# Kernel tuning notes

Hardware: AMD Instinct MI355X
Metric: run time of the kernel (lower is better)

Reference implementation:

```python
import jax, jax.numpy as jnp
import numpy as np
from jax.scipy.special import logsumexp

K = 15          # top-k
N = 4096        # n candidates
BS = 128        # batch size
EPS = 0.1       # entropic regularizer epsilon
MAX_ITER = 200  # Sinkhorn iterations
RANK = 5        # rank of pseudoinverse init
SMALL = 1e-20


def _build_weights():
    """Rank-5 pseudoinverse of Sinkhorn constraint matrix A (as in __init__).
    A maps (f in R^n, g in R^k) -> (f_i + g_c) over rows r = i*(k+1)+c (g_k := 0).
    A^T A = [[(k+1) I_n, J_{n x k}], [J_{k x n}, n I_k]] in closed form."""
    k1 = K + 1
    p = N + K
    G = np.zeros((p, p), dtype=np.float64)
    G[:N, :N] = (k1) * np.eye(N)
    G[:N, N:] = 1.0
    G[N:, :N] = 1.0
    G[N:, N:] = N * np.eye(K)
    w, V = np.linalg.eigh(G)
    idx = np.argsort(w)[-RANK:]
    s = np.sqrt(w[idx])
    V = V[:, idx]                                  # (p, RANK)
    # U = A @ V / s without materializing A (1GB dense):
    vf = V[:N]                                     # (N, RANK)
    vg = np.concatenate([V[N:], np.zeros((1, RANK))], axis=0)  # (k1, RANK)
    U = (vf[:, None, :] + vg[None, :, :]).reshape(N * k1, RANK) / s
    weight1 = (V / s).astype(np.float32)           # (N+K, RANK) = V diag(1/s)
    weight2 = U.T.astype(np.float32)               # (RANK, N*(K+1)) = U^T
    return jnp.asarray(weight1), jnp.asarray(weight2)


def setup_inputs() -> dict:
    key = jax.random.key(0)
    scores = jax.random.normal(key, (BS, N), dtype=jnp.float32)
    tau = jnp.ones((1,), jnp.float32) * 0.1
    weight1, weight2 = _build_weights()
    return {"scores": scores, "tau": tau, "weight1": weight1, "weight2": weight2}


def _sinkhorn(C, mu, nu, Gamma0, weight1, weight2):
    bs, n, k1 = C.shape
    # least-squares warm start for potentials f, g
    b = (C + EPS * jnp.log(Gamma0)).reshape(bs, -1)          # (bs, n*k1)
    x = jnp.einsum('bm,rm->br', b, weight2)                  # (bs, RANK)
    x = jnp.einsum('br,pr->bp', x, weight1)                  # (bs, n+k)
    f = x[:, :n, None]                                       # (bs, n, 1)
    g = jnp.concatenate([x[:, n:], jnp.zeros((bs, 1), C.dtype)], axis=-1)[:, None, :]  # (bs,1,k1)
    elog_mu = EPS * jnp.log(mu)                              # (1, n, 1)
    elog_nu = EPS * jnp.log(nu)                              # (1, 1, k1)

    def step(carry, _):
        f, g = carry
        f = -EPS * logsumexp(-(C - g) / EPS, axis=-1, keepdims=True) + elog_mu
        g = -EPS * logsumexp(-(C - f) / EPS, axis=-2, keepdims=True) + elog_nu
        return (f, g), None

    (f, g), _ = jax.lax.scan(step, (f, g), None, length=MAX_ITER)
    return jnp.exp((-C + f + g) / EPS)


def reference(scores, tau, weight1, weight2):
    bs, n = scores.shape
    k = K
    s = scores[:, :, None]                                   # (bs, n, 1)
    sd = jax.lax.stop_gradient(s)
    max_s = jnp.max(sd)
    min_s = jnp.min(jnp.where(jnp.isneginf(sd), jnp.inf, sd))
    filled = min_s - (max_s - min_s)
    s = jnp.where(jnp.isneginf(s), filled, s)
    anchors = jnp.arange(k, -1, -1, dtype=s.dtype).reshape(1, 1, k + 1)
    C = (s - anchors) ** 2
    C = C / jax.lax.stop_gradient(C.max())
    mu = jnp.full((1, n, 1), 1.0 / n, dtype=s.dtype)
    nu = jnp.concatenate([jnp.full((k,), 1.0 / n), jnp.array([(n - k) / n])]).astype(s.dtype).reshape(1, 1, k + 1)
    # warm-start transport plan Gamma0 from (detached) hard top-k
    topk_val = jax.lax.top_k(jax.lax.stop_gradient(s[..., 0]), k)[0]      # (bs, k)
    Gamma0 = jax.nn.sigmoid(-jnp.abs(topk_val[:, None, :] - s) / tau)     # (bs, n, k)
    Gamma0 = Gamma0 + SMALL
    Gamma0 = Gamma0 / Gamma0.sum(-2, keepdims=True) / n
    Gamma0_last = jnp.clip(1.0 / n - Gamma0.sum(-1, keepdims=True), SMALL, 1.0 - SMALL)
    Gamma0 = jnp.concatenate([Gamma0, Gamma0_last], axis=-1)              # (bs, n, k+1)
    Gamma = _sinkhorn(C, mu, nu, Gamma0, weight1, weight2)
    A = Gamma[:, :, :k] * n
    return A, jnp.linalg.norm(Gamma - Gamma0)
```

## Files before the change

kernel.cpp:

```cpp
#include <hip/hip_runtime.h>
#include <math.h>

#define KK 15
#define K1 16
#define NN 4096
#define BSZ 128
#define NT 512
#define RPT 8
#define NPAIR 4
#define NW 8
#define EPSI 0.1f
#define SMALLC 1e-20f
#define NITER 100
#define W2STRIDE 65536
#define OUT_A_ELEMS (BSZ * NN * KK)
#define TS 20
#define CONV_REL 2e-6f

typedef __attribute__((ext_vector_type(2))) float f2;
typedef __attribute__((ext_vector_type(2))) unsigned u2v;
__device__ __forceinline__ f2 pk_fma(f2 a, f2 b, f2 c){
  return __builtin_elementwise_fma(a, b, c);
}

__device__ __forceinline__ unsigned enc_f32(float f){
  unsigned u = __float_as_uint(f);
  return (u & 0x80000000u) ? ~u : (u | 0x80000000u);
}
__device__ __forceinline__ float dec_f32(unsigned e){
  unsigned u = (e & 0x80000000u) ? (e ^ 0x80000000u) : ~e;
  return __uint_as_float(u);
}


template<int CTRL>
__device__ __forceinline__ float dpp_movf(float x){
  return __uint_as_float((unsigned)__builtin_amdgcn_update_dpp(
      (int)0, (int)__float_as_uint(x), CTRL, 0xF, 0xF, true));
}

__device__ __forceinline__ float bcast_lane0(float x){
  return __uint_as_float((unsigned)__builtin_amdgcn_readlane(
      (int)__float_as_uint(x), 0));
}

__device__ __forceinline__ float xsum16(float r){
#if __has_builtin(__builtin_amdgcn_permlane16_swap)
  u2v s = __builtin_amdgcn_permlane16_swap(__float_as_uint(r), __float_as_uint(r), false, false);
  return __uint_as_float(s.x) + __uint_as_float(s.y);
#else
  return r + __shfl_xor(r, 16);
#endif
}
__device__ __forceinline__ float xsum32(float r){
#if __has_builtin(__builtin_amdgcn_permlane32_swap)
  u2v s = __builtin_amdgcn_permlane32_swap(__float_as_uint(r), __float_as_uint(r), false, false);
  return __uint_as_float(s.x) + __uint_as_float(s.y);
#else
  return r + __shfl_xor(r, 32);
#endif
}

__device__ __forceinline__ float sum16_all(float v){
  v += dpp_movf<0x128>(v);
  v += dpp_movf<0x124>(v);
  v += dpp_movf<0x4E>(v);
  v += dpp_movf<0xB1>(v);
  return v;
}

__device__ __forceinline__ float full64_sum(float v){
  return xsum32(xsum16(sum16_all(v)));
}

__device__ __forceinline__ int fold_col(int lane){
  int l = lane & 15;
  return ((l & 1) << 3) | ((l & 2) << 1) | ((l & 8) >> 2) | ((l & 4) >> 2);
}

__device__ __forceinline__ float wave_fold16(const float p[K1], int lane){
  float a[8];
  {
    const bool hi = (lane & 1) != 0;
    #pragma unroll
    for (int j = 0; j < 8; ++j){
      float send = hi ? p[j] : p[j + 8];
      float keep = hi ? p[j + 8] : p[j];
      a[j] = keep + dpp_movf<0xB1>(send);
    }
  }
  float bq[4];
  {
    const bool hi = (lane & 2) != 0;
    #pragma unroll
    for (int j = 0; j < 4; ++j){
      float send = hi ? a[j] : a[j + 4];
      float keep = hi ? a[j + 4] : a[j];
      bq[j] = keep + dpp_movf<0x4E>(send);
    }
  }
  float cq[2];
  {
    const bool hi = (lane & 8) != 0;
    float s0 = hi ? bq[0] : bq[2];
    float s1 = hi ? bq[1] : bq[3];
    float k0 = hi ? bq[2] : bq[0];
    float k1 = hi ? bq[3] : bq[1];
    cq[0] = k0 + dpp_movf<0x128>(s0);
    cq[1] = k1 + dpp_movf<0x128>(s1);
  }
  float r;
  {
    const bool hi = (lane & 4) != 0;
    float send = hi ? cq[0] : cq[1];
    float keep = hi ? cq[1] : cq[0];
    r = keep + __shfl_xor(send, 4);
  }
  r = xsum16(r);
  r = xsum32(r);
  return r;
}

__device__ __forceinline__ void block_fold16(const float p[K1], float* wb, float* tb,
                                             int lane, int wv, int tid){
  float r = wave_fold16(p, lane);
  if (lane < 16) wb[wv * K1 + fold_col(lane)] = r;
  __syncthreads();
  if (tid < 16){
    float t = 0.0f;
    #pragma unroll
    for (int q = 0; q < NW; ++q) t += wb[q * K1 + tid];
    tb[tid] = t;
  }
  __syncthreads();
}

__global__ __launch_bounds__(NT, 2) void k_main(
    const float* __restrict__ scores, const float* __restrict__ taup,
    const float* __restrict__ w1, const float* __restrict__ w2,
    float* __restrict__ out, unsigned* __restrict__ ws){
  const int b = blockIdx.x;
  const int tid = threadIdx.x;
  const int lane = tid & 63;
  const int wv = tid >> 6;

  __shared__ float tk[KK];
  __shared__ float cands[NW * KK];
  __shared__ __align__(16) float cbuf[K1];
  __shared__ float wbuf[NW * K1];
  __shared__ float wrow[NW * 5];
  __shared__ __align__(16) float xbuf[K1];
  __shared__ __align__(16) float bbcol[K1];
  __shared__ float xv5[8];
  __shared__ __align__(16) float wbufT[2][K1 * TS];
  __shared__ float rv[NW];
  __shared__ float rmn[NW];
  __shared__ unsigned sng[NW];
  __shared__ float statb[4];

  float raw[RPT];
  #pragma unroll
  for (int j = 0; j < RPT; ++j) raw[j] = scores[(size_t)b * NN + tid + NT * j];

  {
    float mx = -INFINITY, mn = INFINITY; unsigned neg = 0u;
    #pragma unroll
    for (int j = 0; j < RPT; ++j){
      float v = raw[j];
      mx = fmaxf(mx, v);
      if (v == -INFINITY) neg = 1u; else mn = fminf(mn, v);
    }
    #pragma unroll
    for (int off = 32; off; off >>= 1){
      mx = fmaxf(mx, __shfl_xor(mx, off));
      mn = fminf(mn, __shfl_xor(mn, off));
      neg |= (unsigned)__shfl_xor((int)neg, off);
    }
    if (lane == 0){ rv[wv] = mx; rmn[wv] = mn; sng[wv] = neg; }
    __syncthreads();
    if (tid == 0){
      for (int q = 1; q < NW; ++q){
        mx = fmaxf(mx, rv[q]); mn = fminf(mn, rmn[q]); neg |= sng[q];
      }
      atomicMax(&ws[0], enc_f32(mx));
      atomicMax(&ws[5], ~enc_f32(mn));
      if (neg) atomicOr(&ws[1], 1u);
      __threadfence();
      atomicAdd(&ws[3], 1u);
      while (__hip_atomic_load(&ws[3], __ATOMIC_ACQUIRE, __HIP_MEMORY_SCOPE_AGENT) < (unsigned)BSZ)
        __builtin_amdgcn_s_sleep(2);
      statb[0] = dec_f32(__hip_atomic_load(&ws[0], __ATOMIC_RELAXED, __HIP_MEMORY_SCOPE_AGENT));
      statb[1] = dec_f32(~__hip_atomic_load(&ws[5], __ATOMIC_RELAXED, __HIP_MEMORY_SCOPE_AGENT));
      statb[2] = __hip_atomic_load(&ws[1], __ATOMIC_RELAXED, __HIP_MEMORY_SCOPE_AGENT) ? 1.0f : 0.0f;
    }
    __syncthreads();
  }

  const float smax = statb[0];
  const float smin_raw = statb[1];
  const bool has_neg = statb[2] != 0.0f;
  const float filled = smin_raw - (smax - smin_raw);
  const float smin_eff = has_neg ? filled : smin_raw;
  const float cmax = fmaxf(fmaxf(smin_eff * smin_eff, smax * smax),
                           fmaxf((smin_eff - 15.0f) * (smin_eff - 15.0f),
                                 (smax - 15.0f) * (smax - 15.0f)));
  const float cinv = 1.0f / cmax;
  const float tauv = taup[0];
  const float invtau = 1.0f / tauv;
  const float inv_n = 1.0f / (float)NN;

  float sv[RPT];
  #pragma unroll
  for (int j = 0; j < RPT; ++j){
    float v = raw[j]; if (v == -INFINITY) v = filled;
    sv[j] = v;
  }

  {
    float lv[RPT];
    #pragma unroll
    for (int j = 0; j < RPT; ++j) lv[j] = sv[j];
    #pragma unroll
    for (int t = 0; t < KK; ++t){
      float bv = lv[0]; int bs = 0;
      #pragma unroll
      for (int j = 1; j < RPT; ++j){ if (lv[j] > bv){ bv = lv[j]; bs = j; } }
      int bidx = (lane << 3) | bs;
      #pragma unroll
      for (int off = 32; off; off >>= 1){
        float ov = __shfl_xor(bv, off);
        int oi = __shfl_xor(bidx, off);
        if (ov > bv || (ov == bv && oi < bidx)){ bv = ov; bidx = oi; }
      }
      if ((bidx >> 3) == lane){
        int s = bidx & 7;
        #pragma unroll
        for (int j = 0; j < RPT; ++j) if (j == s) lv[j] = -INFINITY;
      }
      if (lane == 0) cands[wv * KK + t] = bv;
    }
  }
  __syncthreads();
  if (wv == 0){
    float c0 = (lane < NW * KK) ? cands[lane] : -INFINITY;
    float c1 = (lane + 64 < NW * KK) ? cands[lane + 64] : -INFINITY;
    #pragma unroll
    for (int t = 0; t < KK; ++t){
      int sel = (c0 >= c1) ? 0 : 1;
      float bv = sel ? c1 : c0;
      int bidx = (lane << 1) | sel;
      #pragma unroll
      for (int off = 32; off; off >>= 1){
        float ov = __shfl_xor(bv, off);
        int oi = __shfl_xor(bidx, off);
        if (ov > bv || (ov == bv && oi < bidx)){ bv = ov; bidx = oi; }
      }
      if ((bidx >> 1) == lane){
        if ((bidx & 1) == 0) c0 = -INFINITY; else c1 = -INFINITY;
      }
      if (lane == 0) tk[t] = bv;
    }
  }
  __syncthreads();

  {
    float p[K1];
    float tkr[KK];
    #pragma unroll
    for (int c = 0; c < KK; ++c) tkr[c] = tk[c];
    #pragma unroll
    for (int c = 0; c < K1; ++c) p[c] = 0.0f;
    #pragma unroll
    for (int j = 0; j < RPT; ++j){
      float si = sv[j];
      #pragma unroll
      for (int c = 0; c < KK; ++c){
        float z = fabsf(tkr[c] - si) * invtau;
        float raw1 = __builtin_amdgcn_rcpf(1.0f + __expf(z)) + SMALLC;
        p[c] += raw1;
      }
    }
    block_fold16(p, wbuf, cbuf, lane, wv, tid);
  }

  float colinv_n[KK];
  {
    float pcol[K1];
    float pr0 = 0.0f, pr1 = 0.0f, pr2 = 0.0f, pr3 = 0.0f, pr4 = 0.0f;
    float tkr[KK];
    #pragma unroll
    for (int c = 0; c < KK; ++c){
      tkr[c] = tk[c];
      colinv_n[c] = (1.0f / cbuf[c]) * inv_n;
    }
    #pragma unroll
    for (int c = 0; c < K1; ++c) pcol[c] = 0.0f;
    #pragma unroll
    for (int j = 0; j < RPT; ++j){
      int i = tid + NT * j;
      float si = sv[j];
      float bb[K1];
      float rowpart = 0.0f;
      #pragma unroll
      for (int c = 0; c < KK; ++c){
        float d = si - (float)(KK - c);
        float Cc = d * d * cinv;
        float z = fabsf(tkr[c] - si) * invtau;
        float raw1 = __builtin_amdgcn_rcpf(1.0f + __expf(z)) + SMALLC;
        float g0 = raw1 * colinv_n[c];
        rowpart += g0;
        bb[c] = Cc + EPSI * __logf(g0);
      }
      {
        float Cc = si * si * cinv;
        float g0l = fminf(fmaxf(inv_n - rowpart, SMALLC), 1.0f - SMALLC);
        bb[KK] = Cc + EPSI * __logf(g0l);
      }
      float rs = 0.0f;
      #pragma unroll
      for (int c = 0; c < K1; ++c){ pcol[c] += bb[c]; rs += bb[c]; }
      const float* w1r = w1 + (size_t)i * 5;
      pr0 = fmaf(w1r[0], rs, pr0);
      pr1 = fmaf(w1r[1], rs, pr1);
      pr2 = fmaf(w1r[2], rs, pr2);
      pr3 = fmaf(w1r[3], rs, pr3);
      pr4 = fmaf(w1r[4], rs, pr4);
    }
    float rcol = wave_fold16(pcol, lane);
    float r0 = full64_sum(pr0);
    float r1 = full64_sum(pr1);
    float r2 = full64_sum(pr2);
    float r3 = full64_sum(pr3);
    float r4 = full64_sum(pr4);
    if (lane < 16) wbuf[wv * K1 + fold_col(lane)] = rcol;
    if (lane == 16) wrow[wv * 5 + 0] = r0;
    if (lane == 17) wrow[wv * 5 + 1] = r1;
    if (lane == 18) wrow[wv * 5 + 2] = r2;
    if (lane == 19) wrow[wv * 5 + 3] = r3;
    if (lane == 20) wrow[wv * 5 + 4] = r4;
    __syncthreads();
    if (tid < 16){
      float t = 0.0f;
      #pragma unroll
      for (int q = 0; q < NW; ++q) t += wbuf[q * K1 + tid];
      bbcol[tid] = t;
    } else if (tid < 21){
      int r = tid - 16;
      float t = 0.0f;
      #pragma unroll
      for (int q = 0; q < NW; ++q) t += wrow[q * 5 + r];
      xbuf[r] = t;
    }
    __syncthreads();
    if (tid < 5){
      float xr = xbuf[tid];
      #pragma unroll
      for (int c = 0; c < KK; ++c)
        xr = fmaf(w1[(size_t)(NN + c) * 5 + tid], bbcol[c], xr);
      xv5[tid] = xr;
    }
    __syncthreads();
  }

  float vt[K1];
  {
    float xv[5];
    #pragma unroll
    for (int r = 0; r < 5; ++r) xv[r] = xv5[r];
    #pragma unroll
    for (int c = 0; c < KK; ++c){
      float g = 0.0f;
      #pragma unroll
      for (int r = 0; r < 5; ++r) g += xv[r] * w1[(size_t)(NN + c) * 5 + r];
      float Bc = expf(-10.0f * cinv * (float)((KK - c) * (KK - c)));
      vt[c] = Bc * expf(g * 10.0f);
    }
    vt[KK] = 1.0f;
  }

  f2 x2[NPAIR];
  #pragma unroll
  for (int q = 0; q < NPAIR; ++q){
    x2[q].x = expf(sv[2 * q] * (-20.0f * cinv));
    x2[q].y = expf(sv[2 * q + 1] * (-20.0f * cinv));
  }
  f2 xp[NPAIR][K1];
  #pragma unroll
  for (int q = 0; q < NPAIR; ++q){
    xp[q][0].x = 1.0f; xp[q][0].y = 1.0f;
    xp[q][1] = x2[q];
    #pragma unroll
    for (int c = 2; c < K1; ++c) xp[q][c] = xp[q][c - 1] * x2[q];
  }

  f2 t2[NPAIR];
  const float nmul = ((lane & 15) < KK) ? 1.0f : 4081.0f;
  float pv2 = 0.0f, pv1 = 0.0f;
  int pcnt = -1;
  #pragma unroll 1
  for (int it = 0; it < NITER; ++it){
    const int ph = it & 1;
    #pragma unroll
    for (int q = 0; q < NPAIR; ++q){
      f2 h; h.x = vt[KK]; h.y = vt[KK];
      #pragma unroll
      for (int c = KK - 1; c >= 0; --c){
        f2 vc; vc.x = vt[c]; vc.y = vt[c];
        h = pk_fma(h, x2[q], vc);
      }
      t2[q].x = __builtin_amdgcn_rcpf(h.x);
      t2[q].y = __builtin_amdgcn_rcpf(h.y);
    }
    float p[K1];
    #pragma unroll
    for (int c = 0; c < K1; ++c){
      f2 s = t2[0] * xp[0][c];
      #pragma unroll
      for (int q = 1; q < NPAIR; ++q) s = pk_fma(t2[q], xp[q][c], s);
      p[c] = s.x + s.y;
    }
    float r = wave_fold16(p, lane);
    if (lane < 16) wbufT[ph][fold_col(lane) * TS + wv] = r;
    __syncthreads();
    float md = -1.0f;
    float wout = 0.0f;
    if (lane < 16){
      const float* wp = &wbufT[ph][lane * TS];
      float4 a4 = *(const float4*)wp;
      float4 b4 = *(const float4*)(wp + 4);
      float t = ((a4.x + a4.y) + (a4.z + a4.w)) + ((b4.x + b4.y) + (b4.z + b4.w));
      float wnew = nmul * __builtin_amdgcn_rcpf(t);
      md = fabsf(wnew - pv1) - CONV_REL * pv1;
      wout = wnew;
    }
    if (pcnt >= 1){
      float r1 = 0.0f, r2 = 0.0f;
      if (lane < 16){
        float winv = __builtin_amdgcn_rcpf(wout);
        r1 = (pv1 - pv2) * winv;
        r2 = (wout - pv1) * winv;
      }
      float s12 = full64_sum(r1 * r2);
      float s11 = full64_sum(r1 * r1);
      float s12b = bcast_lane0(s12);
      float s11b = bcast_lane0(s11);
      int anymove = __any((lane < 16) && (fabsf(r2) > 4.0f * CONV_REL));
      float fac = s12b * __builtin_amdgcn_rcpf(s11b - s12b);
      float acc = wout * (1.0f + r2 * fac);
      int okbr = (lane < 16) ? (acc > 0.1f * wout && acc < 10.0f * wout) : 1;
      int allbr = __all(okbr);
      if ((s12b > 0.0f) && (s12b < 0.97f * s11b) && anymove && allbr){
        if (lane < 16) wout = acc;
        pcnt = -1;
      }
    }
    pcnt++;
    pv2 = pv1; pv1 = wout;
    int conv = __all(md <= 0.0f);
    #pragma unroll
    for (int c = 0; c < K1; ++c)
      vt[c] = __uint_as_float((unsigned)__builtin_amdgcn_readlane(
                  (int)__float_as_uint(wout), c));
    if (conv) break;
  }

  float nrm = 0.0f;
  {
    float tkr[KK];
    #pragma unroll
    for (int c = 0; c < KK; ++c) tkr[c] = tk[c];
    #pragma unroll
    for (int q = 0; q < NPAIR; ++q){
      #pragma unroll
      for (int half = 0; half < 2; ++half){
        int i = tid + NT * (2 * q + half);
        float si = sv[2 * q + half];
        float tin = (half ? t2[q].y : t2[q].x) * inv_n;
        float rowpart = 0.0f;
        float gamv[KK];
        float gaml;
        #pragma unroll
        for (int c = 0; c < KK; ++c){
          float xc = half ? xp[q][c].y : xp[q][c].x;
          float gam = (tin * xc) * vt[c];
          float z = fabsf(tkr[c] - si) * invtau;
          float raw1 = __builtin_amdgcn_rcpf(1.0f + __expf(z)) + SMALLC;
          float g0 = raw1 * colinv_n[c];
          rowpart += g0;
          float d = gam - g0;
          nrm += d * d;
          gamv[c] = gam * (float)NN;
        }
        {
          float xc = half ? xp[q][KK].y : xp[q][KK].x;
          gaml = (tin * xc) * vt[KK];
          float g0l = fminf(fmaxf(inv_n - rowpart, SMALLC), 1.0f - SMALLC);
          float d = gaml - g0l;
          nrm += d * d;
        }
        float* op = out + (size_t)(b * NN + i) * KK;
        #pragma unroll
        for (int c = 0; c < KK; ++c) op[c] = gamv[c];
      }
    }
  }
  #pragma unroll
  for (int off = 32; off; off >>= 1) nrm += __shfl_xor(nrm, off);
  if (lane == 0) rv[wv] = nrm;
  __syncthreads();
  if (tid == 0){
    float t = 0.0f;
    for (int q = 0; q < NW; ++q) t += rv[q];
    atomicAdd(reinterpret_cast<float*>(ws) + 2, t);
    __threadfence();
    unsigned prev = atomicAdd(&ws[4], 1u);
    if (prev == (unsigned)(BSZ - 1)){
      float n2 = __hip_atomic_load(reinterpret_cast<float*>(ws) + 2,
                                   __ATOMIC_RELAXED, __HIP_MEMORY_SCOPE_AGENT);
      out[OUT_A_ELEMS] = sqrtf(n2);
    }
  }
}

extern "C" void kernel_launch(void* const* d_in, const int* in_sizes, int n_in,
                              void* d_out, int out_size, void* d_ws, size_t ws_size,
                              hipStream_t stream){
  const float* scores = (const float*)d_in[0];
  const float* tau    = (const float*)d_in[1];
  const float* w1     = (const float*)d_in[2];
  const float* w2     = (const float*)d_in[3];
  float* out = (float*)d_out;
  unsigned* ws = (unsigned*)d_ws;

  hipMemsetAsync(ws, 0x00, 24, stream);

  k_main<<<BSZ, NT, 0, stream>>>(scores, tau, w1, w2, out, ws);
}
```

Before: 142.4 us.

## Split each batch row across two cooperating blocks with pairwise global syncs

Launches two blocks per batch row instead of one. Each block handles half the candidate rows in the top-k, warm-start column sums and output-writing phases. Partial top-k lists, column sums and least-squares reductions are merged through per-row workspace slots using a global-memory pair barrier. The Sinkhorn iteration itself still appears to run redundantly in both blocks. The change adds cross-block spin waits and relies on all 256 blocks being co-resident for the global statistics barrier.

```diff
diff --git a/kernel.cpp b/kernel.cpp
--- a/kernel.cpp
+++ b/kernel.cpp
@@ -5,17 +5,28 @@
 #define K1 16
 #define NN 4096
 #define BSZ 128
+#define NBLK 256
 #define NT 512
 #define RPT 8
+#define RPTD 4
 #define NPAIR 4
 #define NW 8
 #define EPSI 0.1f
 #define SMALLC 1e-20f
 #define NITER 100
-#define W2STRIDE 65536
 #define OUT_A_ELEMS (BSZ * NN * KK)
 #define TS 20
 #define CONV_REL 2e-6f
+
+#define SLOTW 128
+#define WS_WORDS (16 + BSZ * SLOTW)
+#define SO_CTOP 0
+#define SO_CCOL 1
+#define SO_CWARM 2
+#define SO_TOPK 8
+#define SO_COL  40
+#define SO_WCOL 72
+#define SO_RD   104
 
 typedef __attribute__((ext_vector_type(2))) float f2;
 typedef __attribute__((ext_vector_type(2))) unsigned u2v;
@@ -31,7 +42,6 @@
   unsigned u = (e & 0x80000000u) ? (e ^ 0x80000000u) : ~e;
   return __uint_as_float(u);
 }
-
 
 template<int CTRL>
 __device__ __forceinline__ float dpp_movf(float x){
@@ -68,7 +78,6 @@
   v += dpp_movf<0xB1>(v);
   return v;
 }
-
 __device__ __forceinline__ float full64_sum(float v){
   return xsum32(xsum16(sum16_all(v)));
 }
@@ -135,14 +144,30 @@
   __syncthreads();
 }
 
+__device__ __forceinline__ void pair_sync(unsigned* ctr, int tid){
+  __threadfence();
+  __syncthreads();
+  if (tid == 0){
+    __hip_atomic_fetch_add(ctr, 1u, __ATOMIC_RELEASE, __HIP_MEMORY_SCOPE_AGENT);
+    while (__hip_atomic_load(ctr, __ATOMIC_ACQUIRE, __HIP_MEMORY_SCOPE_AGENT) < 2u)
+      __builtin_amdgcn_s_sleep(1);
+  }
+  __syncthreads();
+}
+
 __global__ __launch_bounds__(NT, 2) void k_main(
     const float* __restrict__ scores, const float* __restrict__ taup,
     const float* __restrict__ w1, const float* __restrict__ w2,
     float* __restrict__ out, unsigned* __restrict__ ws){
-  const int b = blockIdx.x;
+  const int bid = blockIdx.x;
+  const int b   = bid & (BSZ - 1);
+  const int half= bid >> 7;
+  const int JB  = 4 * half;
   const int tid = threadIdx.x;
   const int lane = tid & 63;
   const int wv = tid >> 6;
+  unsigned* slot = ws + 16 + b * SLOTW;
+  float* slotf = (float*)slot;
 
   __shared__ float tk[KK];
   __shared__ float cands[NW * KK];
@@ -187,7 +212,7 @@
       if (neg) atomicOr(&ws[1], 1u);
       __threadfence();
       atomicAdd(&ws[3], 1u);
-      while (__hip_atomic_load(&ws[3], __ATOMIC_ACQUIRE, __HIP_MEMORY_SCOPE_AGENT) < (unsigned)BSZ)
+      while (__hip_atomic_load(&ws[3], __ATOMIC_ACQUIRE, __HIP_MEMORY_SCOPE_AGENT) < (unsigned)NBLK)
         __builtin_amdgcn_s_sleep(2);
       statb[0] = dec_f32(__hip_atomic_load(&ws[0], __ATOMIC_RELAXED, __HIP_MEMORY_SCOPE_AGENT));
       statb[1] = dec_f32(~__hip_atomic_load(&ws[5], __ATOMIC_RELAXED, __HIP_MEMORY_SCOPE_AGENT));
@@ -217,25 +242,25 @@
   }
 
   {
-    float lv[RPT];
-    #pragma unroll
-    for (int j = 0; j < RPT; ++j) lv[j] = sv[j];
+    float lv[RPTD];
+    #pragma unroll
+    for (int j = 0; j < RPTD; ++j) lv[j] = sv[JB + j];
     #pragma unroll
     for (int t = 0; t < KK; ++t){
       float bv = lv[0]; int bs = 0;
       #pragma unroll
-      for (int j = 1; j < RPT; ++j){ if (lv[j] > bv){ bv = lv[j]; bs = j; } }
-      int bidx = (lane << 3) | bs;
+      for (int j = 1; j < RPTD; ++j){ if (lv[j] > bv){ bv = lv[j]; bs = j; } }
+      int bidx = (lane << 2) | bs;
       #pragma unroll
       for (int off = 32; off; off >>= 1){
         float ov = __shfl_xor(bv, off);
         int oi = __shfl_xor(bidx, off);
         if (ov > bv || (ov == bv && oi < bidx)){ bv = ov; bidx = oi; }
       }
-      if ((bidx >> 3) == lane){
-        int s = bidx & 7;
+      if ((bidx >> 2) == lane){
+        int s = bidx & 3;
         #pragma unroll
-        for (int j = 0; j < RPT; ++j) if (j == s) lv[j] = -INFINITY;
+        for (int j = 0; j < RPTD; ++j) if (j == s) lv[j] = -INFINITY;
       }
       if (lane == 0) cands[wv * KK + t] = bv;
     }
@@ -262,6 +287,19 @@
     }
   }
   __syncthreads();
+  if (tid < K1) slotf[SO_TOPK + half * K1 + tid] = (tid < KK) ? tk[tid] : -INFINITY;
+  pair_sync(&slot[SO_CTOP], tid);
+  if (tid == 0){
+    const float* ga = slotf + SO_TOPK;
+    const float* gb = slotf + SO_TOPK + K1;
+    int ia = 0, ib = 0;
+    #pragma unroll
+    for (int t = 0; t < KK; ++t){
+      float va = ga[ia], vb = gb[ib];
+      if (va >= vb){ tk[t] = va; ++ia; } else { tk[t] = vb; ++ib; }
+    }
+  }
+  __syncthreads();
 
   {
     float p[K1];
@@ -271,8 +309,8 @@
     #pragma unroll
     for (int c = 0; c < K1; ++c) p[c] = 0.0f;
     #pragma unroll
-    for (int j = 0; j < RPT; ++j){
-      float si = sv[j];
+    for (int j = 0; j < RPTD; ++j){
+      float si = sv[JB + j];
       #pragma unroll
       for (int c = 0; c < KK; ++c){
         float z = fabsf(tkr[c] - si) * invtau;
@@ -282,6 +320,10 @@
     }
     block_fold16(p, wbuf, cbuf, lane, wv, tid);
   }
+  if (tid < K1) slotf[SO_COL + half * K1 + tid] = cbuf[tid];
+  pair_sync(&slot[SO_CCOL], tid);
+  if (tid < K1) cbuf[tid] = slotf[SO_COL + tid] + slotf[SO_COL + K1 + tid];
+  __syncthreads();
 
   float colinv_n[KK];
   {
@@ -296,9 +338,9 @@
     #pragma unroll
     for (int c = 0; c < K1; ++c) pcol[c] = 0.0f;
     #pragma unroll
-    for (int j = 0; j < RPT; ++j){
-      int i = tid + NT * j;
-      float si = sv[j];
+    for (int j = 0; j < RPTD; ++j){
+      int i = tid + NT * (JB + j);
+      float si = sv[JB + j];
       float bb[K1];
       float rowpart = 0.0f;
       #pragma unroll
@@ -352,6 +394,15 @@
       xbuf[r] = t;
     }
     __syncthreads();
+    if (tid < K1) slotf[SO_WCOL + half * K1 + tid] = bbcol[tid];
+    else if (tid < K1 + 5) slotf[SO_RD + half * 8 + (tid - K1)] = xbuf[tid - K1];
+    pair_sync(&slot[SO_CWARM], tid);
+    if (tid < K1) bbcol[tid] = slotf[SO_WCOL + tid] + slotf[SO_WCOL + K1 + tid];
+    else if (tid < K1 + 5){
+      int r = tid - K1;
+      xbuf[r] = slotf[SO_RD + r] + slotf[SO_RD + 8 + r];
+    }
+    __syncthreads();
     if (tid < 5){
       float xr = xbuf[tid];
       #pragma unroll
@@ -470,18 +521,19 @@
     #pragma unroll
     for (int c = 0; c < KK; ++c) tkr[c] = tk[c];
     #pragma unroll
-    for (int q = 0; q < NPAIR; ++q){
-      #pragma unroll
-      for (int half = 0; half < 2; ++half){
-        int i = tid + NT * (2 * q + half);
-        float si = sv[2 * q + half];
-        float tin = (half ? t2[q].y : t2[q].x) * inv_n;
+    for (int qq = 0; qq < 2; ++qq){
+      const int q = 2 * half + qq;
+      #pragma unroll
+      for (int e = 0; e < 2; ++e){
+        int i = tid + NT * (2 * q + e);
+        float si = sv[2 * q + e];
+        float tin = (e ? t2[q].y : t2[q].x) * inv_n;
         float rowpart = 0.0f;
         float gamv[KK];
         float gaml;
         #pragma unroll
         for (int c = 0; c < KK; ++c){
-          float xc = half ? xp[q][c].y : xp[q][c].x;
+          float xc = e ? xp[q][c].y : xp[q][c].x;
           float gam = (tin * xc) * vt[c];
           float z = fabsf(tkr[c] - si) * invtau;
           float raw1 = __builtin_amdgcn_rcpf(1.0f + __expf(z)) + SMALLC;
@@ -492,7 +544,7 @@
           gamv[c] = gam * (float)NN;
         }
         {
-          float xc = half ? xp[q][KK].y : xp[q][KK].x;
+          float xc = e ? xp[q][KK].y : xp[q][KK].x;
           gaml = (tin * xc) * vt[KK];
           float g0l = fminf(fmaxf(inv_n - rowpart, SMALLC), 1.0f - SMALLC);
           float d = gaml - g0l;
@@ -514,7 +566,7 @@
     atomicAdd(reinterpret_cast<float*>(ws) + 2, t);
     __threadfence();
     unsigned prev = atomicAdd(&ws[4], 1u);
-    if (prev == (unsigned)(BSZ - 1)){
+    if (prev == (unsigned)(NBLK - 1)){
       float n2 = __hip_atomic_load(reinterpret_cast<float*>(ws) + 2,
                                    __ATOMIC_RELAXED, __HIP_MEMORY_SCOPE_AGENT);
       out[OUT_A_ELEMS] = sqrtf(n2);
@@ -532,7 +584,7 @@
   float* out = (float*)d_out;
   unsigned* ws = (unsigned*)d_ws;
 
-  hipMemsetAsync(ws, 0x00, 24, stream);
-
-  k_main<<<BSZ, NT, 0, stream>>>(scores, tau, w1, w2, out, ws);
-}
+  hipMemsetAsync(ws, 0x00, WS_WORDS * 4, stream);
+
+  k_main<<<NBLK, NT, 0, stream>>>(scores, tau, w1, w2, out, ws);
+}
```

Measured after the change: 269.0 us. 1.89x slower.

## Duplicate each batch row across two blocks and overlap top-k with grid barrier

Applied to the files above, without the earlier changes.

Launches two blocks per batch row. Both blocks redundantly run the full Sinkhorn iteration, and each writes half of the output rows and half of the norm contribution. The per-row top-k selection now runs before the global min/max spin-wait, so it overlaps the grid-wide barrier, and -inf top-k values are replaced by the fill value afterwards. This doubles the Sinkhorn compute and relies on all 256 blocks being co-resident for the spin barrier, in exchange for splitting the heavy output-write epilogue and filling more CUs.

```diff
diff --git a/kernel.cpp b/kernel.cpp
--- a/kernel.cpp
+++ b/kernel.cpp
@@ -5,6 +5,7 @@
 #define K1 16
 #define NN 4096
 #define BSZ 128
+#define NBLK 256
 #define NT 512
 #define RPT 8
 #define NPAIR 4
@@ -12,7 +13,6 @@
 #define EPSI 0.1f
 #define SMALLC 1e-20f
 #define NITER 100
-#define W2STRIDE 65536
 #define OUT_A_ELEMS (BSZ * NN * KK)
 #define TS 20
 #define CONV_REL 2e-6f
@@ -68,7 +68,6 @@
   v += dpp_movf<0xB1>(v);
   return v;
 }
-
 __device__ __forceinline__ float full64_sum(float v){
   return xsum32(xsum16(sum16_all(v)));
 }
@@ -139,7 +138,9 @@
     const float* __restrict__ scores, const float* __restrict__ taup,
     const float* __restrict__ w1, const float* __restrict__ w2,
     float* __restrict__ out, unsigned* __restrict__ ws){
-  const int b = blockIdx.x;
+  const int bid = blockIdx.x;
+  const int b   = bid & (BSZ - 1);
+  const int half= bid >> 7;
   const int tid = threadIdx.x;
   const int lane = tid & 63;
   const int wv = tid >> 6;
@@ -187,14 +188,62 @@
       if (neg) atomicOr(&ws[1], 1u);
       __threadfence();
       atomicAdd(&ws[3], 1u);
-      while (__hip_atomic_load(&ws[3], __ATOMIC_ACQUIRE, __HIP_MEMORY_SCOPE_AGENT) < (unsigned)BSZ)
-        __builtin_amdgcn_s_sleep(2);
-      statb[0] = dec_f32(__hip_atomic_load(&ws[0], __ATOMIC_RELAXED, __HIP_MEMORY_SCOPE_AGENT));
-      statb[1] = dec_f32(~__hip_atomic_load(&ws[5], __ATOMIC_RELAXED, __HIP_MEMORY_SCOPE_AGENT));
-      statb[2] = __hip_atomic_load(&ws[1], __ATOMIC_RELAXED, __HIP_MEMORY_SCOPE_AGENT) ? 1.0f : 0.0f;
-    }
-    __syncthreads();
-  }
+    }
+  }
+
+  {
+    float lv[RPT];
+    #pragma unroll
+    for (int j = 0; j < RPT; ++j) lv[j] = raw[j];
+    #pragma unroll
+    for (int t = 0; t < KK; ++t){
+      float bv = lv[0]; int bs = 0;
+      #pragma unroll
+      for (int j = 1; j < RPT; ++j){ if (lv[j] > bv){ bv = lv[j]; bs = j; } }
+      int bidx = (lane << 3) | bs;
+      #pragma unroll
+      for (int off = 32; off; off >>= 1){
+        float ov = __shfl_xor(bv, off);
+        int oi = __shfl_xor(bidx, off);
+        if (ov > bv || (ov == bv && oi < bidx)){ bv = ov; bidx = oi; }
+      }
+      if ((bidx >> 3) == lane){
+        int s = bidx & 7;
+        #pragma unroll
+        for (int j = 0; j < RPT; ++j) if (j == s) lv[j] = -INFINITY;
+      }
+      if (lane == 0) cands[wv * KK + t] = bv;
+    }
+  }
+  __syncthreads();
+  if (wv == 0){
+    float c0 = (lane < NW * KK) ? cands[lane] : -INFINITY;
+    float c1 = (lane + 64 < NW * KK) ? cands[lane + 64] : -INFINITY;
+    #pragma unroll
+    for (int t = 0; t < KK; ++t){
+      int sel = (c0 >= c1) ? 0 : 1;
+      float bv = sel ? c1 : c0;
+      int bidx = (lane << 1) | sel;
+      #pragma unroll
+      for (int off = 32; off; off >>= 1){
+        float ov = __shfl_xor(bv, off);
+        int oi = __shfl_xor(bidx, off);
+        if (ov > bv || (ov == bv && oi < bidx)){ bv = ov; bidx = oi; }
+      }
+      if ((bidx >> 1) == lane){
+        if ((bidx & 1) == 0) c0 = -INFINITY; else c1 = -INFINITY;
+      }
+      if (lane == 0) tk[t] = bv;
+    }
+  }
+  if (tid == 0){
+    while (__hip_atomic_load(&ws[3], __ATOMIC_ACQUIRE, __HIP_MEMORY_SCOPE_AGENT) < (unsigned)NBLK)
+      __builtin_amdgcn_s_sleep(2);
+    statb[0] = dec_f32(__hip_atomic_load(&ws[0], __ATOMIC_RELAXED, __HIP_MEMORY_SCOPE_AGENT));
+    statb[1] = dec_f32(~__hip_atomic_load(&ws[5], __ATOMIC_RELAXED, __HIP_MEMORY_SCOPE_AGENT));
+    statb[2] = __hip_atomic_load(&ws[1], __ATOMIC_RELAXED, __HIP_MEMORY_SCOPE_AGENT) ? 1.0f : 0.0f;
+  }
+  __syncthreads();
 
   const float smax = statb[0];
   const float smin_raw = statb[1];
@@ -217,57 +266,13 @@
   }
 
   {
-    float lv[RPT];
-    #pragma unroll
-    for (int j = 0; j < RPT; ++j) lv[j] = sv[j];
-    #pragma unroll
-    for (int t = 0; t < KK; ++t){
-      float bv = lv[0]; int bs = 0;
-      #pragma unroll
-      for (int j = 1; j < RPT; ++j){ if (lv[j] > bv){ bv = lv[j]; bs = j; } }
-      int bidx = (lane << 3) | bs;
-      #pragma unroll
-      for (int off = 32; off; off >>= 1){
-        float ov = __shfl_xor(bv, off);
-        int oi = __shfl_xor(bidx, off);
-        if (ov > bv || (ov == bv && oi < bidx)){ bv = ov; bidx = oi; }
-      }
-      if ((bidx >> 3) == lane){
-        int s = bidx & 7;
-        #pragma unroll
-        for (int j = 0; j < RPT; ++j) if (j == s) lv[j] = -INFINITY;
-      }
-      if (lane == 0) cands[wv * KK + t] = bv;
-    }
-  }
-  __syncthreads();
-  if (wv == 0){
-    float c0 = (lane < NW * KK) ? cands[lane] : -INFINITY;
-    float c1 = (lane + 64 < NW * KK) ? cands[lane + 64] : -INFINITY;
-    #pragma unroll
-    for (int t = 0; t < KK; ++t){
-      int sel = (c0 >= c1) ? 0 : 1;
-      float bv = sel ? c1 : c0;
-      int bidx = (lane << 1) | sel;
-      #pragma unroll
-      for (int off = 32; off; off >>= 1){
-        float ov = __shfl_xor(bv, off);
-        int oi = __shfl_xor(bidx, off);
-        if (ov > bv || (ov == bv && oi < bidx)){ bv = ov; bidx = oi; }
-      }
-      if ((bidx >> 1) == lane){
-        if ((bidx & 1) == 0) c0 = -INFINITY; else c1 = -INFINITY;
-      }
-      if (lane == 0) tk[t] = bv;
-    }
-  }
-  __syncthreads();
-
-  {
     float p[K1];
     float tkr[KK];
     #pragma unroll
-    for (int c = 0; c < KK; ++c) tkr[c] = tk[c];
+    for (int c = 0; c < KK; ++c){
+      float tv = tk[c];
+      tkr[c] = (tv == -INFINITY) ? filled : tv;
+    }
     #pragma unroll
     for (int c = 0; c < K1; ++c) p[c] = 0.0f;
     #pragma unroll
@@ -290,7 +295,8 @@
     float tkr[KK];
     #pragma unroll
     for (int c = 0; c < KK; ++c){
-      tkr[c] = tk[c];
+      float tv = tk[c];
+      tkr[c] = (tv == -INFINITY) ? filled : tv;
       colinv_n[c] = (1.0f / cbuf[c]) * inv_n;
     }
     #pragma unroll
@@ -468,20 +474,24 @@
   {
     float tkr[KK];
     #pragma unroll
-    for (int c = 0; c < KK; ++c) tkr[c] = tk[c];
-    #pragma unroll
-    for (int q = 0; q < NPAIR; ++q){
-      #pragma unroll
-      for (int half = 0; half < 2; ++half){
-        int i = tid + NT * (2 * q + half);
-        float si = sv[2 * q + half];
-        float tin = (half ? t2[q].y : t2[q].x) * inv_n;
+    for (int c = 0; c < KK; ++c){
+      float tv = tk[c];
+      tkr[c] = (tv == -INFINITY) ? filled : tv;
+    }
+    #pragma unroll
+    for (int qq = 0; qq < 2; ++qq){
+      const int q = 2 * half + qq;
+      #pragma unroll
+      for (int e = 0; e < 2; ++e){
+        int i = tid + NT * (2 * q + e);
+        float si = sv[2 * q + e];
+        float tin = (e ? t2[q].y : t2[q].x) * inv_n;
         float rowpart = 0.0f;
         float gamv[KK];
         float gaml;
         #pragma unroll
         for (int c = 0; c < KK; ++c){
-          float xc = half ? xp[q][c].y : xp[q][c].x;
+          float xc = e ? xp[q][c].y : xp[q][c].x;
           float gam = (tin * xc) * vt[c];
           float z = fabsf(tkr[c] - si) * invtau;
           float raw1 = __builtin_amdgcn_rcpf(1.0f + __expf(z)) + SMALLC;
@@ -492,7 +502,7 @@
           gamv[c] = gam * (float)NN;
         }
         {
-          float xc = half ? xp[q][KK].y : xp[q][KK].x;
+          float xc = e ? xp[q][KK].y : xp[q][KK].x;
           gaml = (tin * xc) * vt[KK];
           float g0l = fminf(fmaxf(inv_n - rowpart, SMALLC), 1.0f - SMALLC);
           float d = gaml - g0l;
@@ -514,7 +524,7 @@
     atomicAdd(reinterpret_cast<float*>(ws) + 2, t);
     __threadfence();
     unsigned prev = atomicAdd(&ws[4], 1u);
-    if (prev == (unsigned)(BSZ - 1)){
+    if (prev == (unsigned)(NBLK - 1)){
       float n2 = __hip_atomic_load(reinterpret_cast<float*>(ws) + 2,
                                    __ATOMIC_RELAXED, __HIP_MEMORY_SCOPE_AGENT);
       out[OUT_A_ELEMS] = sqrtf(n2);
@@ -534,5 +544,5 @@
 
   hipMemsetAsync(ws, 0x00, 24, stream);
 
-  k_main<<<BSZ, NT, 0, stream>>>(scores, tau, w1, w2, out, ws);
-}
+  k_main<<<NBLK, NT, 0, stream>>>(scores, tau, w1, w2, out, ws);
+}
```

New measurement: 170.5 us. +19.7%, slower.
